# Kernel tuning notes

Hardware: AMD Instinct MI355X
Metric: run time of the kernel (lower is better)

## Reference

```python
import jax, jax.numpy as jnp
import numpy as np

L, N, HID, HEADS, BLK = 4096, 2, 1024, 16, 64
RAND_NUM = 2


def setup_inputs() -> dict:
    key = jax.random.key(0)
    ks = jax.random.split(key, 11)
    s = 0.02
    nb = L // BLK
    return {
        "query": jax.random.normal(ks[0], (L, N, HID), jnp.float32),
        "q_proj": jax.random.normal(ks[1], (HID, HID), jnp.float32) * s,
        "q_bias": jax.random.normal(ks[2], (HID,), jnp.float32) * s,
        "k_proj": jax.random.normal(ks[3], (HID, HID), jnp.float32) * s,
        "k_bias": jax.random.normal(ks[4], (HID,), jnp.float32) * s,
        "v_proj": jax.random.normal(ks[5], (HID, HID), jnp.float32) * s,
        "v_bias": jax.random.normal(ks[6], (HID,), jnp.float32) * s,
        "out_proj": jax.random.normal(ks[7], (HID, HID), jnp.float32) * s,
        "out_bias": jax.random.normal(ks[8], (HID,), jnp.float32) * s,
        "rand_indices": jax.random.randint(ks[9], (nb - 2, RAND_NUM), 2, nb, jnp.int64 if jax.config.jax_enable_x64 else jnp.int32),
        "h": HEADS,
        "block_size": BLK,
    }


def reference(query, q_proj, q_bias, k_proj, k_bias, v_proj, v_bias,
              out_proj, out_bias, rand_indices, h, block_size):
    Lq, Nb, hidden = query.shape
    dh = hidden // h
    b = block_size
    nb = Lq // b
    Z = Nb * h  # batch*heads leading dim
    scale = dh ** -0.5

    lin = lambda x, w, bi: x @ w.T + bi
    # [L, N, hidden] -> [N*h, L, dh]
    q = lin(query, q_proj, q_bias).reshape(Lq, Z, dh).transpose(1, 0, 2) * scale
    k = lin(query, k_proj, k_bias).reshape(Lq, Z, dh).transpose(1, 0, 2)
    v = lin(query, v_proj, v_bias).reshape(Lq, Z, dh).transpose(1, 0, 2)

    qb = q.reshape(Z, nb, b, dh)
    kb = k.reshape(Z, nb, b, dh)
    vb = v.reshape(Z, nb, b, dh)

    # ---- global blocks: first 2 blocks of queries attend to everything;
    #      all middle queries attend to first 2 key blocks ----
    head = jnp.einsum('zqd,zkd->zqk', q[:, :2 * b], k)          # [Z, 2b, L]
    col = jnp.einsum('zqd,zkd->zqk', q[:, 2 * b:], k[:, :2 * b])  # [Z, L-2b, 2b]

    # ---- sliding window (3 neighboring blocks), bottom row zero-padded ----
    skeys = jnp.concatenate([kb[:, 1:-2], kb[:, 2:-1], kb[:, 3:]], axis=2)  # [Z, nb-3, 3b, dh]
    sbot_k = jnp.concatenate([jnp.zeros_like(kb[:, -1:]), kb[:, -2:-1], kb[:, -1:]], axis=2)
    skeys = jnp.concatenate([skeys, sbot_k], axis=1)            # [Z, nb-2, 3b, dh]
    sqk = jnp.einsum('znqd,znkd->znqk', qb[:, 2:], skeys)
    sqk = sqk.reshape(Z, (nb - 2) * b, 3 * b)

    # ---- random blocks (rand_num per query block) ----
    gk = kb[:, rand_indices].reshape(Z, nb - 2, RAND_NUM * b, dh)
    rqk = jnp.einsum('znqd,znkd->znqk', qb[:, 2:], gk)
    rqk = rqk.reshape(Z, (nb - 2) * b, RAND_NUM * b)

    middle = jnp.concatenate([col, sqk, rqk], axis=-1)          # [Z, L-2b, 7b]

    head_attn = jax.nn.softmax(head, axis=-1)
    mid_attn = jax.nn.softmax(middle, axis=-1)

    # ---- attn @ v ----
    head_out = jnp.einsum('zqk,zkd->zqd', head_attn, v)          # [Z, 2b, dh]
    mid_out = jnp.einsum('zqk,zkd->zqd', mid_attn[:, :, :2 * b], v[:, :2 * b])

    svals = jnp.concatenate([vb[:, 1:-2], vb[:, 2:-1], vb[:, 3:]], axis=2)
    sbot_v = jnp.concatenate([vb[:, -2:-1], vb[:, -1:], jnp.zeros_like(vb[:, -1:])], axis=2)
    svals = jnp.concatenate([svals, sbot_v], axis=1)             # [Z, nb-2, 3b, dh]
    ms = mid_attn[:, :, 2 * b:5 * b].reshape(Z, nb - 2, b, 3 * b)
    mid_out = mid_out + jnp.einsum('znqk,znkd->znqd', ms, svals).reshape(Z, (nb - 2) * b, dh)

    gv = vb[:, rand_indices].reshape(Z, nb - 2, RAND_NUM * b, dh)
    mr = mid_attn[:, :, 5 * b:].reshape(Z, nb - 2, b, RAND_NUM * b)
    mid_out = mid_out + jnp.einsum('znqk,znkd->znqd', mr, gv).reshape(Z, (nb - 2) * b, dh)

    out = jnp.concatenate([head_out, mid_out], axis=1)           # [Z, L, dh]
    out = out.transpose(1, 0, 2).reshape(Lq, Nb, hidden)
    return lin(out, out_proj, out_bias)
```

## Files before the change

kernel.cpp:

```cpp
#include <hip/hip_runtime.h>
#include <stdint.h>

#define L_SEQ 4096
#define NBATCH 2
#define HID 1024
#define HEADS 16
#define DH 64
#define Z_DIM 32
#define NBLK 64
#define NROWS 8192
#define NSPLIT 8

typedef float f32x4 __attribute__((ext_vector_type(4)));
typedef short short8 __attribute__((ext_vector_type(8)));
typedef uint32_t u32x4 __attribute__((ext_vector_type(4)));

typedef const uint32_t __attribute__((address_space(1))) *gas_ptr;
typedef uint32_t __attribute__((address_space(3))) *las_ptr;

__device__ __forceinline__ ushort f2bf(float f) {
  uint32_t u = __float_as_uint(f);
  uint32_t r = (u + 0x7FFFu + ((u >> 16) & 1u)) >> 16;
  return (ushort)r;
}

__device__ __forceinline__ uint32_t cvtpk(float a, float b) {
  uint32_t r;
  asm("v_cvt_pk_bf16_f32 %0, %1, %2" : "=v"(r) : "v"(a), "v"(b));
  return r;
}

__device__ __forceinline__ void gload_lds16(const void* g, void* l) {
  __builtin_amdgcn_global_load_lds((gas_ptr)g, (las_ptr)l, 16, 0, 0);
}

__global__ __launch_bounds__(256)
void cvt_multi(const float* __restrict__ s0, ushort* __restrict__ d0,
               const float* __restrict__ s1, ushort* __restrict__ d1,
               const float* __restrict__ s2, ushort* __restrict__ d2,
               const float* __restrict__ s3, ushort* __restrict__ d3,
               const float* __restrict__ s4, ushort* __restrict__ d4) {
  const int i = blockIdx.x * blockDim.x + threadIdx.x;
  const int NQ = NROWS * HID / 4;
  const float4* src; ushort4* dst; int off;
  if (i < NQ) {
    src = (const float4*)s0; dst = (ushort4*)d0; off = i;
  } else {
    const int j = i - NQ;
    const int r = j >> 18;
    off = j & ((1 << 18) - 1);
    src = (const float4*)(r == 0 ? s1 : r == 1 ? s2 : r == 2 ? s3 : s4);
    dst = (ushort4*)(r == 0 ? d1 : r == 1 ? d2 : r == 2 ? d3 : d4);
  }
  float4 v = src[off];
  ushort4 o;
  o.x = f2bf(v.x); o.y = f2bf(v.y); o.z = f2bf(v.z); o.w = f2bf(v.w);
  dst[off] = o;
}

template <int FINAL>
__global__ __launch_bounds__(256)
void gemm_bt(const ushort* __restrict__ X,
             const ushort* __restrict__ W0, const ushort* __restrict__ W1,
             const ushort* __restrict__ W2,
             const float* __restrict__ b0, const float* __restrict__ b1,
             const float* __restrict__ b2,
             ushort* __restrict__ Qo, ushort* __restrict__ Ko,
             ushort* __restrict__ Vo, float* __restrict__ Fo) {
  const int tid = threadIdx.x;
  const int w = tid >> 6, l = tid & 63;
  const int lr = l & 15, lg = l >> 4;
  const int wr = w >> 1, wc = w & 1;

  const int total = FINAL ? 512 : 1536;
  const int per = total >> 3;
  const int f0 = blockIdx.x;
  const int nf = (f0 & 7) * per + (f0 >> 3);
  const int bx = nf & 7;
  const int by = (nf >> 3) & 63;
  const int zid = FINAL ? 0 : (nf >> 9);
  const int mbase = by * 128;
  const int nbase = bx * 128;

  const ushort* W = FINAL ? W0 : (zid == 0 ? W0 : (zid == 1 ? W1 : W2));
  const float*  B = FINAL ? b0 : (zid == 0 ? b0 : (zid == 1 ? b1 : b2));

  __shared__ ushort lds[3][8192];

  const int kch = (lg ^ ((lr >> 1) & 3)) << 3;

  f32x4 acc[4][4];
#pragma unroll
  for (int m = 0; m < 4; ++m)
#pragma unroll
    for (int n = 0; n < 4; ++n) acc[m][n] = (f32x4){0.f, 0.f, 0.f, 0.f};

  auto stage = [&](int k0, int buf) {
#pragma unroll
    for (int s = 0; s < 2; ++s) {
      const int chunk = s * 256 + tid;
      const int row = chunk >> 2, cc = chunk & 3;
      const int scc = cc ^ ((row >> 1) & 3);
      gload_lds16(X + (size_t)(mbase + row) * HID + k0 + scc * 8,
                  &lds[buf][(s * 256 + (tid & ~63)) * 8]);
      gload_lds16(W + (size_t)(nbase + row) * HID + k0 + scc * 8,
                  &lds[buf][4096 + (s * 256 + (tid & ~63)) * 8]);
    }
  };

  auto compute_tile = [&](const ushort* lA, const ushort* lB) {
    short8 af[4], bfr[4];
#pragma unroll
    for (int m = 0; m < 4; ++m)
      af[m] = *(const short8*)&lA[(wr * 64 + m * 16 + lr) * 32 + kch];
#pragma unroll
    for (int n = 0; n < 4; ++n)
      bfr[n] = *(const short8*)&lB[(wc * 64 + n * 16 + lr) * 32 + kch];
#pragma unroll
    for (int m = 0; m < 4; ++m)
#pragma unroll
      for (int n = 0; n < 4; ++n)
        acc[m][n] = __builtin_amdgcn_mfma_f32_16x16x32_bf16(af[m], bfr[n], acc[m][n], 0, 0, 0);
  };

  stage(0, 0);
  stage(32, 1);
  for (int t = 0; t < 32; ++t) {
    if (t < 30) { asm volatile("s_waitcnt vmcnt(4)" ::: "memory"); }
    else        { asm volatile("s_waitcnt vmcnt(0)" ::: "memory"); }
    __builtin_amdgcn_s_barrier();
    __builtin_amdgcn_sched_barrier(0);
    const int b = t % 3;
    compute_tile(&lds[b][0], &lds[b][4096]);
    if (t < 30) stage((t + 2) * 32, (t + 2) % 3);
  }

  if (FINAL) {
#pragma unroll
    for (int n = 0; n < 4; ++n) {
      const int col = nbase + wc * 64 + n * 16 + lr;
      const float bias = B[col];
#pragma unroll
      for (int m = 0; m < 4; ++m)
#pragma unroll
        for (int r = 0; r < 4; ++r) {
          const int row = mbase + wr * 64 + m * 16 + 4 * lg + r;
          Fo[(size_t)row * HID + col] = acc[m][n][r] + bias;
        }
    }
    return;
  }

  float biasn[4];
#pragma unroll
  for (int n = 0; n < 4; ++n) biasn[n] = B[nbase + wc * 64 + n * 16 + lr];
  ushort* st = &lds[0][0];

  if (zid == 2) {
#pragma unroll
    for (int nb2 = 0; nb2 < 2; ++nb2) {
#pragma unroll
      for (int ch = 0; ch < 2; ++ch) {
        __syncthreads();
        if (wc == ch) {
#pragma unroll
          for (int m = 0; m < 4; ++m)
#pragma unroll
            for (int n = 0; n < 4; ++n)
#pragma unroll
              for (int rr = 0; rr < 2; ++rr) {
                const int r = nb2 + 2 * rr;
                st[(n * 16 + lr) * 72 + wr * 32 + m * 8 + 2 * lg + rr] =
                    f2bf(acc[m][n][r] + biasn[n]);
              }
        }
        __syncthreads();
        const int zz = nb2 * HEADS + (nbase >> 6) + ch;
#pragma unroll
        for (int it = 0; it < 2; ++it) {
          const int c = it * 256 + tid;
          const int colI = c >> 3, ls0 = (c & 7) * 8;
          const short8 v = *(const short8*)&st[colI * 72 + ls0];
          *(short8*)&Vo[((size_t)zz * DH + colI) * L_SEQ + (mbase >> 1) + ls0] = v;
        }
      }
    }
  } else {
    ushort* Out = (zid == 0) ? Qo : Ko;
    const float sc = (zid == 0) ? 0.125f : 1.f;
#pragma unroll
    for (int nbp = 0; nbp < 2; ++nbp) {
#pragma unroll
      for (int hh = 0; hh < 2; ++hh) {
        __syncthreads();
        if (wc == hh) {
#pragma unroll
          for (int m = 0; m < 4; ++m)
#pragma unroll
            for (int n = 0; n < 4; ++n)
#pragma unroll
              for (int rr = 0; rr < 2; ++rr) {
                const int r = nbp + 2 * rr;
                st[(wr * 32 + m * 8 + 2 * lg + rr) * 72 + n * 16 + lr] =
                    f2bf((acc[m][n][r] + biasn[n]) * sc);
              }
        }
        __syncthreads();
        const int zz = nbp * HEADS + (nbase >> 6) + hh;
#pragma unroll
        for (int it = 0; it < 2; ++it) {
          const int c = it * 256 + tid;
          const int lr2 = c >> 3, cc8 = c & 7;
          const short8 v = *(const short8*)&st[lr2 * 72 + cc8 * 8];
          *(short8*)&Out[((size_t)zz * L_SEQ + (mbase >> 1) + lr2) * DH + cc8 * 8] = v;
        }
      }
    }
  }
}

__global__ __launch_bounds__(256)
void attn_sparse(const ushort* __restrict__ Q, const ushort* __restrict__ K,
                 const ushort* __restrict__ Vt, const int* __restrict__ rnd,
                 ushort* __restrict__ O,
                 float* __restrict__ Pp, float* __restrict__ Mp,
                 float* __restrict__ Lp) {
  const int bid = blockIdx.x;
  int z, qb, split = 0;
  bool head;
  if (bid < Z_DIM * 62) {
    const int x = bid & 7, k = bid >> 3;
    z = x * 4 + k / 62;
    qb = 2 + k % 62;
    head = false;
  } else {
    const int t = bid - Z_DIM * 62;
    const int x = t & 7, j = t >> 3;
    z = x * 4 + (j & 3);
    const int s2 = j >> 2;
    qb = s2 & 1;
    split = s2 >> 1;
    head = true;
  }
  const int tid = threadIdx.x;
  const int w = tid >> 6, l = tid & 63;
  const int lr = l & 15, lg = l >> 4;

  __shared__ ushort Kl[64 * 64];
  __shared__ ushort Vl[64 * 64];
  __shared__ uint32_t P2[4][16 * 36];

  const ushort* Qrow = Q + ((size_t)z * L_SEQ + qb * 64 + w * 16 + lr) * DH;
  const short8 bq0 = *(const short8*)(Qrow + lg * 8);
  const short8 bq1 = *(const short8*)(Qrow + 32 + lg * 8);

  float m = -1e30f, lsum = 0.f;
  f32x4 accO[4];
#pragma unroll
  for (int td = 0; td < 4; ++td) accO[td] = (f32x4){0.f, 0.f, 0.f, 0.f};

  const int nslot = head ? 8 : 7;
  int sk[3] = {0, 0, 0}, sv[3] = {0, 0, 0}, rk0 = 0, rk1 = 0;
  if (!head) {
    const int i = qb - 2;
    rk0 = rnd[2 * i]; rk1 = rnd[2 * i + 1];
    if (qb < NBLK - 1) {
      sk[0] = qb - 1; sk[1] = qb; sk[2] = qb + 1;
      sv[0] = qb - 1; sv[1] = qb; sv[2] = qb + 1;
    } else {
      sk[0] = -1; sk[1] = NBLK - 2; sk[2] = NBLK - 1;
      sv[0] = NBLK - 2; sv[1] = NBLK - 1; sv[2] = -1;
    }
  }

  for (int slot = 0; slot < nslot; ++slot) {
    int ki, vi;
    if (head) { ki = split * 8 + slot; vi = ki; }
    else if (slot < 2) { ki = slot; vi = slot; }
    else if (slot < 5) { ki = sk[slot - 2]; vi = sv[slot - 2]; }
    else { ki = (slot == 5) ? rk0 : rk1; vi = ki; }

    if (slot) __syncthreads();
#pragma unroll
    for (int s = 0; s < 2; ++s) {
      const int chunk = s * 256 + tid;
      const int row = chunk >> 3, cc = chunk & 7;
      const int scc = cc ^ (row & 7);
      if (ki >= 0)
        gload_lds16(K + ((size_t)z * L_SEQ + ki * 64 + row) * DH + scc * 8,
                    &Kl[(s * 256 + (tid & ~63)) * 8]);
      if (vi >= 0)
        gload_lds16(Vt + ((size_t)z * DH + row) * L_SEQ + vi * 64 + scc * 8,
                    &Vl[(s * 256 + (tid & ~63)) * 8]);
    }
    __syncthreads();

    f32x4 sc[4];
    if (ki >= 0) {
      __builtin_amdgcn_s_setprio(1);
#pragma unroll
      for (int t = 0; t < 4; ++t) {
        const int row = t * 16 + lr;
        const short8 a0 = *(const short8*)&Kl[row * 64 + ((lg ^ (row & 7)) << 3)];
        const short8 a1 = *(const short8*)&Kl[row * 64 + (((4 + lg) ^ (row & 7)) << 3)];
        f32x4 zz = (f32x4){0.f, 0.f, 0.f, 0.f};
        sc[t] = __builtin_amdgcn_mfma_f32_16x16x32_bf16(a0, bq0, zz, 0, 0, 0);
        sc[t] = __builtin_amdgcn_mfma_f32_16x16x32_bf16(a1, bq1, sc[t], 0, 0, 0);
      }
      __builtin_amdgcn_s_setprio(0);
    } else {
#pragma unroll
      for (int t = 0; t < 4; ++t) sc[t] = (f32x4){0.f, 0.f, 0.f, 0.f};
    }

    float sm = sc[0][0];
#pragma unroll
    for (int t = 0; t < 4; ++t)
#pragma unroll
      for (int r = 0; r < 4; ++r) sm = fmaxf(sm, sc[t][r]);
    sm = fmaxf(sm, __shfl_xor(sm, 16));
    sm = fmaxf(sm, __shfl_xor(sm, 32));
    const float mn = fmaxf(m, sm);
    const float scale = __expf(m - mn);
    m = mn;
    lsum *= scale;
#pragma unroll
    for (int td = 0; td < 4; ++td)
#pragma unroll
      for (int r = 0; r < 4; ++r) accO[td][r] *= scale;
    float psum = 0.f;
#pragma unroll
    for (int t = 0; t < 4; ++t)
#pragma unroll
      for (int r = 0; r < 4; ++r) {
        const float p = __expf(sc[t][r] - mn);
        sc[t][r] = p;
        psum += p;
      }
    psum += __shfl_xor(psum, 16);
    psum += __shfl_xor(psum, 32);
    lsum += psum;

    if (vi >= 0) {
      uint32_t* Pq = &P2[w][0];
#pragma unroll
      for (int t = 0; t < 4; ++t) {
        Pq[lr * 36 + t * 8 + 2 * lg + 0] = cvtpk(sc[t][0], sc[t][1]);
        Pq[lr * 36 + t * 8 + 2 * lg + 1] = cvtpk(sc[t][2], sc[t][3]);
      }
      union { u32x4 u; short8 s8; } pb0, pb1;
      pb0.u = *(const u32x4*)&Pq[lr * 36 + lg * 4];
      pb1.u = *(const u32x4*)&Pq[lr * 36 + 16 + lg * 4];
      __builtin_amdgcn_s_setprio(1);
#pragma unroll
      for (int td = 0; td < 4; ++td) {
        const int row = td * 16 + lr;
        const short8 av0 = *(const short8*)&Vl[row * 64 + ((lg ^ (row & 7)) << 3)];
        const short8 av1 = *(const short8*)&Vl[row * 64 + (((4 + lg) ^ (row & 7)) << 3)];
        accO[td] = __builtin_amdgcn_mfma_f32_16x16x32_bf16(av0, pb0.s8, accO[td], 0, 0, 0);
        accO[td] = __builtin_amdgcn_mfma_f32_16x16x32_bf16(av1, pb1.s8, accO[td], 0, 0, 0);
      }
      __builtin_amdgcn_s_setprio(0);
    }
  }

  if (!head) {
    const float inv = 1.f / lsum;
    const int nb = z >> 4, hd = z & 15;
    const size_t rowbase =
        ((size_t)(qb * 64 + w * 16 + lr) * NBATCH + nb) * HID + hd * 64;
#pragma unroll
    for (int td = 0; td < 4; ++td) {
      uint2 o;
      o.x = cvtpk(accO[td][0] * inv, accO[td][1] * inv);
      o.y = cvtpk(accO[td][2] * inv, accO[td][3] * inv);
      *(uint2*)&O[rowbase + td * 16 + 4 * lg] = o;
    }
  } else {
    const int hbase = (qb * Z_DIM + z) * NSPLIT + split;
    const size_t prow = (size_t)hbase * 64 + w * 16 + lr;
#pragma unroll
    for (int td = 0; td < 4; ++td)
      *(f32x4*)&Pp[prow * 64 + td * 16 + 4 * lg] = accO[td];
    if (l < 16) {
      Mp[hbase * 64 + w * 16 + lr] = m;
      Lp[hbase * 64 + w * 16 + lr] = lsum;
    }
  }
}

__global__ __launch_bounds__(256)
void head_reduce(const float* __restrict__ Pp, const float* __restrict__ Mp,
                 const float* __restrict__ Lp, ushort* __restrict__ O) {
  const int z = blockIdx.x >> 1, qb = blockIdx.x & 1;
  const int tid = threadIdx.x;
  const int row = tid >> 2, cg = tid & 3;
  const int base = (qb * Z_DIM + z) * NSPLIT;

  float mm[NSPLIT], wgt[NSPLIT];
  float mx = -1e30f;
#pragma unroll
  for (int s = 0; s < NSPLIT; ++s) {
    mm[s] = Mp[(base + s) * 64 + row];
    mx = fmaxf(mx, mm[s]);
  }
  float denom = 0.f;
#pragma unroll
  for (int s = 0; s < NSPLIT; ++s) {
    wgt[s] = __expf(mm[s] - mx);
    denom += Lp[(base + s) * 64 + row] * wgt[s];
  }
  const float inv = 1.f / denom;

  const int nb = z >> 4, hd = z & 15;
  const int lseq = qb * 64 + row;
#pragma unroll
  for (int c = 0; c < 16; ++c) {
    const int col = cg * 16 + c;
    float acc = 0.f;
#pragma unroll
    for (int s = 0; s < NSPLIT; ++s)
      acc += Pp[((size_t)(base + s) * 64 + row) * 64 + col] * wgt[s];
    O[((size_t)lseq * NBATCH + nb) * HID + hd * 64 + col] = f2bf(acc * inv);
  }
}

extern "C" void kernel_launch(void* const* d_in, const int* in_sizes, int n_in,
                              void* d_out, int out_size, void* d_ws, size_t ws_size,
                              hipStream_t stream) {
  (void)in_sizes; (void)n_in; (void)out_size; (void)ws_size;
  const float* query    = (const float*)d_in[0];
  const float* q_proj   = (const float*)d_in[1];
  const float* q_bias   = (const float*)d_in[2];
  const float* k_proj   = (const float*)d_in[3];
  const float* k_bias   = (const float*)d_in[4];
  const float* v_proj   = (const float*)d_in[5];
  const float* v_bias   = (const float*)d_in[6];
  const float* out_proj = (const float*)d_in[7];
  const float* out_bias = (const float*)d_in[8];
  const int*   rnd      = (const int*)d_in[9];

  ushort* Xb  = (ushort*)d_ws;
  ushort* Wq  = Xb + (size_t)NROWS * HID;
  ushort* Wk  = Wq + (size_t)HID * HID;
  ushort* Wv  = Wk + (size_t)HID * HID;
  ushort* Wo  = Wv + (size_t)HID * HID;
  ushort* Qb  = Wo + (size_t)HID * HID;
  ushort* Kb  = Qb + (size_t)Z_DIM * L_SEQ * DH;
  ushort* Vtb = Kb + (size_t)Z_DIM * L_SEQ * DH;
  float*  Pp  = (float*)(Vtb + (size_t)Z_DIM * DH * L_SEQ);
  float*  Mp  = Pp + (size_t)2 * Z_DIM * NSPLIT * 64 * 64;
  float*  Lp  = Mp + (size_t)2 * Z_DIM * NSPLIT * 64;
  ushort* Ob  = Xb;
  float*  Fo  = (float*)d_out;

  cvt_multi<<<(NROWS * HID / 4 + 4 * HID * HID / 4) / 256, 256, 0, stream>>>(
      query, Xb, q_proj, Wq, k_proj, Wk, v_proj, Wv, out_proj, Wo);

  gemm_bt<0><<<1536, 256, 0, stream>>>(
      Xb, Wq, Wk, Wv, q_bias, k_bias, v_bias, Qb, Kb, Vtb, nullptr);

  attn_sparse<<<Z_DIM * 62 + 2 * Z_DIM * NSPLIT, 256, 0, stream>>>(
      Qb, Kb, Vtb, rnd, Ob, Pp, Mp, Lp);

  head_reduce<<<2 * Z_DIM, 256, 0, stream>>>(Pp, Mp, Lp, Ob);

  gemm_bt<1><<<512, 256, 0, stream>>>(
      Ob, Wo, nullptr, nullptr, out_bias, nullptr, nullptr,
      nullptr, nullptr, nullptr, Fo);
}
```

Before: 154.6 us.

## Process two query blocks per attention workgroup to share staged K/V tiles

Each middle-region workgroup now handles two adjacent query blocks, so the global key blocks and overlapping sliding-window K/V tiles are staged once into LDS and used for both. Stages drop from 14 to 10 per pair, which cuts global-to-LDS traffic and barrier count, and the grid for that part is halved. In exchange it uses more registers for the two accumulator sets, runs fewer workgroups, and needs a special schedule for the last block pair where the padded zero-key block and the shifted value block come into play.

```diff
diff --git a/kernel.cpp b/kernel.cpp
--- a/kernel.cpp
+++ b/kernel.cpp
@@ -226,20 +226,20 @@
                  float* __restrict__ Pp, float* __restrict__ Mp,
                  float* __restrict__ Lp) {
   const int bid = blockIdx.x;
-  int z, qb, split = 0;
+  int z, p = 0, qb0 = 0, qb1 = 0, split = 0, qbh = 0;
   bool head;
-  if (bid < Z_DIM * 62) {
+  if (bid < Z_DIM * 31) {
     const int x = bid & 7, k = bid >> 3;
-    z = x * 4 + k / 62;
-    qb = 2 + k % 62;
+    z = x * 4 + k / 31;
+    p = k % 31;
+    qb0 = 2 + 2 * p; qb1 = qb0 + 1;
     head = false;
   } else {
-    const int t = bid - Z_DIM * 62;
+    const int t = bid - Z_DIM * 31;
     const int x = t & 7, j = t >> 3;
     z = x * 4 + (j & 3);
     const int s2 = j >> 2;
-    qb = s2 & 1;
-    split = s2 >> 1;
+    qbh = s2 & 1; split = s2 >> 1;
     head = true;
   }
   const int tid = threadIdx.x;
@@ -250,53 +250,45 @@
   __shared__ ushort Vl[64 * 64];
   __shared__ uint32_t P2[4][16 * 36];
 
-  const ushort* Qrow = Q + ((size_t)z * L_SEQ + qb * 64 + w * 16 + lr) * DH;
-  const short8 bq0 = *(const short8*)(Qrow + lg * 8);
-  const short8 bq1 = *(const short8*)(Qrow + 32 + lg * 8);
-
-  float m = -1e30f, lsum = 0.f;
-  f32x4 accO[4];
-#pragma unroll
-  for (int td = 0; td < 4; ++td) accO[td] = (f32x4){0.f, 0.f, 0.f, 0.f};
-
-  const int nslot = head ? 8 : 7;
-  int sk[3] = {0, 0, 0}, sv[3] = {0, 0, 0}, rk0 = 0, rk1 = 0;
+  const int qrow0 = head ? qbh : qb0;
+  const ushort* Qr0 = Q + ((size_t)z * L_SEQ + qrow0 * 64 + w * 16 + lr) * DH;
+  short8 bq0[2], bq1[2];
+  bq0[0] = *(const short8*)(Qr0 + lg * 8);
+  bq1[0] = *(const short8*)(Qr0 + 32 + lg * 8);
   if (!head) {
-    const int i = qb - 2;
-    rk0 = rnd[2 * i]; rk1 = rnd[2 * i + 1];
-    if (qb < NBLK - 1) {
-      sk[0] = qb - 1; sk[1] = qb; sk[2] = qb + 1;
-      sv[0] = qb - 1; sv[1] = qb; sv[2] = qb + 1;
-    } else {
-      sk[0] = -1; sk[1] = NBLK - 2; sk[2] = NBLK - 1;
-      sv[0] = NBLK - 2; sv[1] = NBLK - 1; sv[2] = -1;
-    }
-  }
-
-  for (int slot = 0; slot < nslot; ++slot) {
-    int ki, vi;
-    if (head) { ki = split * 8 + slot; vi = ki; }
-    else if (slot < 2) { ki = slot; vi = slot; }
-    else if (slot < 5) { ki = sk[slot - 2]; vi = sv[slot - 2]; }
-    else { ki = (slot == 5) ? rk0 : rk1; vi = ki; }
-
-    if (slot) __syncthreads();
+    const ushort* Qr1 = Q + ((size_t)z * L_SEQ + qb1 * 64 + w * 16 + lr) * DH;
+    bq0[1] = *(const short8*)(Qr1 + lg * 8);
+    bq1[1] = *(const short8*)(Qr1 + 32 + lg * 8);
+  } else {
+    bq0[1] = bq0[0]; bq1[1] = bq1[0];
+  }
+
+  float m2[2] = {-1e30f, -1e30f}, ls[2] = {0.f, 0.f};
+  f32x4 accO[2][4];
+#pragma unroll
+  for (int q = 0; q < 2; ++q)
+#pragma unroll
+    for (int td = 0; td < 4; ++td) accO[q][td] = (f32x4){0.f, 0.f, 0.f, 0.f};
+
+  auto stage = [&](int ki, int vi) {
 #pragma unroll
     for (int s = 0; s < 2; ++s) {
       const int chunk = s * 256 + tid;
       const int row = chunk >> 3, cc = chunk & 7;
       const int scc = cc ^ (row & 7);
-      if (ki >= 0)
-        gload_lds16(K + ((size_t)z * L_SEQ + ki * 64 + row) * DH + scc * 8,
-                    &Kl[(s * 256 + (tid & ~63)) * 8]);
-      if (vi >= 0)
-        gload_lds16(Vt + ((size_t)z * DH + row) * L_SEQ + vi * 64 + scc * 8,
-                    &Vl[(s * 256 + (tid & ~63)) * 8]);
-    }
-    __syncthreads();
-
+      gload_lds16(K + ((size_t)z * L_SEQ + ki * 64 + row) * DH + scc * 8,
+                  &Kl[(s * 256 + (tid & ~63)) * 8]);
+      gload_lds16(Vt + ((size_t)z * DH + row) * L_SEQ + vi * 64 + scc * 8,
+                  &Vl[(s * 256 + (tid & ~63)) * 8]);
+    }
+  };
+
+  auto process = [&](const int q, const int code) {
     f32x4 sc[4];
-    if (ki >= 0) {
+    if (code == 2) {
+#pragma unroll
+      for (int t = 0; t < 4; ++t) sc[t] = (f32x4){0.f, 0.f, 0.f, 0.f};
+    } else {
       __builtin_amdgcn_s_setprio(1);
 #pragma unroll
       for (int t = 0; t < 4; ++t) {
@@ -304,13 +296,10 @@
         const short8 a0 = *(const short8*)&Kl[row * 64 + ((lg ^ (row & 7)) << 3)];
         const short8 a1 = *(const short8*)&Kl[row * 64 + (((4 + lg) ^ (row & 7)) << 3)];
         f32x4 zz = (f32x4){0.f, 0.f, 0.f, 0.f};
-        sc[t] = __builtin_amdgcn_mfma_f32_16x16x32_bf16(a0, bq0, zz, 0, 0, 0);
-        sc[t] = __builtin_amdgcn_mfma_f32_16x16x32_bf16(a1, bq1, sc[t], 0, 0, 0);
+        sc[t] = __builtin_amdgcn_mfma_f32_16x16x32_bf16(a0, bq0[q], zz, 0, 0, 0);
+        sc[t] = __builtin_amdgcn_mfma_f32_16x16x32_bf16(a1, bq1[q], sc[t], 0, 0, 0);
       }
       __builtin_amdgcn_s_setprio(0);
-    } else {
-#pragma unroll
-      for (int t = 0; t < 4; ++t) sc[t] = (f32x4){0.f, 0.f, 0.f, 0.f};
     }
 
     float sm = sc[0][0];
@@ -320,28 +309,28 @@
       for (int r = 0; r < 4; ++r) sm = fmaxf(sm, sc[t][r]);
     sm = fmaxf(sm, __shfl_xor(sm, 16));
     sm = fmaxf(sm, __shfl_xor(sm, 32));
-    const float mn = fmaxf(m, sm);
-    const float scale = __expf(m - mn);
-    m = mn;
-    lsum *= scale;
+    const float mn = fmaxf(m2[q], sm);
+    const float scale = __expf(m2[q] - mn);
+    m2[q] = mn;
+    ls[q] *= scale;
 #pragma unroll
     for (int td = 0; td < 4; ++td)
 #pragma unroll
-      for (int r = 0; r < 4; ++r) accO[td][r] *= scale;
+      for (int r = 0; r < 4; ++r) accO[q][td][r] *= scale;
     float psum = 0.f;
 #pragma unroll
     for (int t = 0; t < 4; ++t)
 #pragma unroll
       for (int r = 0; r < 4; ++r) {
-        const float p = __expf(sc[t][r] - mn);
-        sc[t][r] = p;
-        psum += p;
+        const float pv = __expf(sc[t][r] - mn);
+        sc[t][r] = pv;
+        psum += pv;
       }
     psum += __shfl_xor(psum, 16);
     psum += __shfl_xor(psum, 32);
-    lsum += psum;
-
-    if (vi >= 0) {
+    ls[q] += psum;
+
+    if (code != 3) {
       uint32_t* Pq = &P2[w][0];
 #pragma unroll
       for (int t = 0; t < 4; ++t) {
@@ -357,34 +346,72 @@
         const int row = td * 16 + lr;
         const short8 av0 = *(const short8*)&Vl[row * 64 + ((lg ^ (row & 7)) << 3)];
         const short8 av1 = *(const short8*)&Vl[row * 64 + (((4 + lg) ^ (row & 7)) << 3)];
-        accO[td] = __builtin_amdgcn_mfma_f32_16x16x32_bf16(av0, pb0.s8, accO[td], 0, 0, 0);
-        accO[td] = __builtin_amdgcn_mfma_f32_16x16x32_bf16(av1, pb1.s8, accO[td], 0, 0, 0);
+        accO[q][td] = __builtin_amdgcn_mfma_f32_16x16x32_bf16(av0, pb0.s8, accO[q][td], 0, 0, 0);
+        accO[q][td] = __builtin_amdgcn_mfma_f32_16x16x32_bf16(av1, pb1.s8, accO[q][td], 0, 0, 0);
       }
       __builtin_amdgcn_s_setprio(0);
     }
+  };
+
+  const int nround = head ? NSPLIT : 10;
+  for (int r = 0; r < nround; ++r) {
+    int kb, vb, code0, code1;
+    if (head) {
+      kb = vb = split * 8 + r; code0 = 1; code1 = 0;
+    } else if (r < 2) {
+      kb = vb = r; code0 = 1; code1 = 1;
+    } else if (r >= 6) {
+      const bool forQ1 = (r >= 8);
+      const int ii = forQ1 ? (qb1 - 2) : (qb0 - 2);
+      kb = vb = rnd[2 * ii + (r & 1)];
+      code0 = forQ1 ? 0 : 1;
+      code1 = forQ1 ? 1 : 0;
+    } else {
+      if (p < 30) {
+        kb = vb = qb0 - 3 + r;
+        code0 = (r < 5) ? 1 : 0;
+        code1 = (r > 2) ? 1 : 0;
+      } else {
+        if (r == 2)      { kb = 61; vb = 61; code0 = 1; code1 = 0; }
+        else if (r == 3) { kb = 62; vb = 62; code0 = 1; code1 = 2; }
+        else if (r == 4) { kb = 62; vb = 63; code0 = 0; code1 = 1; }
+        else             { kb = 63; vb = 63; code0 = 1; code1 = 3; }
+      }
+    }
+
+    if (r) __syncthreads();
+    stage(kb, vb);
+    __syncthreads();
+
+    if (code0) process(0, code0);
+    if (code1) process(1, code1);
   }
 
   if (!head) {
-    const float inv = 1.f / lsum;
     const int nb = z >> 4, hd = z & 15;
-    const size_t rowbase =
-        ((size_t)(qb * 64 + w * 16 + lr) * NBATCH + nb) * HID + hd * 64;
-#pragma unroll
-    for (int td = 0; td < 4; ++td) {
-      uint2 o;
-      o.x = cvtpk(accO[td][0] * inv, accO[td][1] * inv);
-      o.y = cvtpk(accO[td][2] * inv, accO[td][3] * inv);
-      *(uint2*)&O[rowbase + td * 16 + 4 * lg] = o;
+#pragma unroll
+    for (int q = 0; q < 2; ++q) {
+      const float inv = 1.f / ls[q];
+      const int qq = q ? qb1 : qb0;
+      const size_t rowbase =
+          ((size_t)(qq * 64 + w * 16 + lr) * NBATCH + nb) * HID + hd * 64;
+#pragma unroll
+      for (int td = 0; td < 4; ++td) {
+        uint2 o;
+        o.x = cvtpk(accO[q][td][0] * inv, accO[q][td][1] * inv);
+        o.y = cvtpk(accO[q][td][2] * inv, accO[q][td][3] * inv);
+        *(uint2*)&O[rowbase + td * 16 + 4 * lg] = o;
+      }
     }
   } else {
-    const int hbase = (qb * Z_DIM + z) * NSPLIT + split;
+    const int hbase = (qbh * Z_DIM + z) * NSPLIT + split;
     const size_t prow = (size_t)hbase * 64 + w * 16 + lr;
 #pragma unroll
     for (int td = 0; td < 4; ++td)
-      *(f32x4*)&Pp[prow * 64 + td * 16 + 4 * lg] = accO[td];
+      *(f32x4*)&Pp[prow * 64 + td * 16 + 4 * lg] = accO[0][td];
     if (l < 16) {
-      Mp[hbase * 64 + w * 16 + lr] = m;
-      Lp[hbase * 64 + w * 16 + lr] = lsum;
+      Mp[hbase * 64 + w * 16 + lr] = m2[0];
+      Lp[hbase * 64 + w * 16 + lr] = ls[0];
     }
   }
 }
@@ -460,7 +487,7 @@
   gemm_bt<0><<<1536, 256, 0, stream>>>(
       Xb, Wq, Wk, Wv, q_bias, k_bias, v_bias, Qb, Kb, Vtb, nullptr);
 
-  attn_sparse<<<Z_DIM * 62 + 2 * Z_DIM * NSPLIT, 256, 0, stream>>>(
+  attn_sparse<<<Z_DIM * 31 + 2 * Z_DIM * NSPLIT, 256, 0, stream>>>(
       Qb, Kb, Vtb, rnd, Ob, Pp, Mp, Lp);
 
   head_reduce<<<2 * Z_DIM, 256, 0, stream>>>(Pp, Mp, Lp, Ob);
```

After: 155.6 us. Within noise of the previous version (+0.7%).

## Replace QKV projection GEMM with 256x256-tile, 8-wave pipelined kernel

Applied to the files above, without the earlier changes.

Adds a dedicated QKV projection kernel that uses 256x256 output tiles with 512 threads, a 64-wide K step split into two halves, and an 8-buffer LDS ring. Global-to-LDS loads are interleaved with MFMA phases, with setprio hints and explicit waitcnt/barrier scheduling. The larger tile raises arithmetic intensity and reuse of A and B per LDS load, and cuts the grid from 1536 to 384 blocks. In exchange it needs 128 KB of LDS per block and more accumulator registers, which lowers occupancy and leaves fewer blocks to balance across CUs. The old generic gemm_bt loses its QKV path and is kept only for the output projection.

```diff
diff --git a/kernel.cpp b/kernel.cpp
--- a/kernel.cpp
+++ b/kernel.cpp
@@ -58,32 +58,206 @@
   dst[off] = o;
 }
 
+#define VM4 asm volatile("s_waitcnt vmcnt(4)" ::: "memory")
+#define VMNOP
+
+#define GP(DBUF, KH, MLO, STG, VM)                                          \
+  {                                                                         \
+    const ushort* sA_ = &lds8[(DBUF) * 4 + (KH) * 2][0];                    \
+    const ushort* sB_ = &lds8[(DBUF) * 4 + (KH) * 2 + 1][0];                \
+    short8 af_[4], bf_[4];                                                  \
+    _Pragma("unroll")                                                       \
+    for (int mm = 0; mm < 4; ++mm)                                          \
+      af_[mm] = *(const short8*)&sA_[aoff + ((MLO) + mm) * 512];            \
+    _Pragma("unroll")                                                       \
+    for (int nn = 0; nn < 4; ++nn)                                          \
+      bf_[nn] = *(const short8*)&sB_[boff + nn * 512];                      \
+    STG;                                                                    \
+    VM;                                                                     \
+    __builtin_amdgcn_s_barrier();                                           \
+    asm volatile("s_waitcnt lgkmcnt(0)" ::: "memory");                      \
+    __builtin_amdgcn_sched_barrier(0);                                      \
+    __builtin_amdgcn_s_setprio(1);                                          \
+    _Pragma("unroll")                                                       \
+    for (int mm = 0; mm < 4; ++mm)                                          \
+      _Pragma("unroll")                                                     \
+      for (int nn = 0; nn < 4; ++nn)                                        \
+        acc[(MLO) + mm][nn] = __builtin_amdgcn_mfma_f32_16x16x32_bf16(      \
+            af_[mm], bf_[nn], acc[(MLO) + mm][nn], 0, 0, 0);                \
+    __builtin_amdgcn_s_setprio(0);                                          \
+    __builtin_amdgcn_s_barrier();                                           \
+  }
+
+__global__ __launch_bounds__(512)
+void gemm_qkv256(const ushort* __restrict__ X,
+                 const ushort* __restrict__ W0, const ushort* __restrict__ W1,
+                 const ushort* __restrict__ W2,
+                 const float* __restrict__ b0, const float* __restrict__ b1,
+                 const float* __restrict__ b2,
+                 ushort* __restrict__ Qo, ushort* __restrict__ Ko,
+                 ushort* __restrict__ Vo) {
+  const int tid = threadIdx.x;
+  const int w = tid >> 6, l = tid & 63;
+  const int lr = l & 15, lg = l >> 4;
+  const int wr = w >> 2, wc = w & 3;
+
+  const int f0 = blockIdx.x;
+  const int nf = (f0 & 7) * 48 + (f0 >> 3);
+  const int bx = nf & 3;
+  const int by = (nf >> 2) & 31;
+  const int zid = nf >> 7;
+  const int mbase = by * 256;
+  const int nbase = bx * 256;
+
+  const ushort* W = (zid == 0) ? W0 : (zid == 1 ? W1 : W2);
+  const float*  Bb = (zid == 0) ? b0 : (zid == 1 ? b1 : b2);
+
+  __shared__ ushort lds8[8][8192];
+
+  int srow[2], skc[2];
+#pragma unroll
+  for (int c = 0; c < 2; ++c) {
+    const int idx = c * 512 + tid;
+    const int rp = idx >> 3;
+    const int cs = (idx & 7) ^ (rp & 7);
+    srow[c] = rp * 2 + (cs >> 2);
+    skc[c] = (cs & 3) * 8;
+  }
+  const int dst0 = (tid & ~63) * 8;
+  const int dst1 = (512 + (tid & ~63)) * 8;
+
+  auto stA = [&](int dbuf, int kh, int kt) {
+    ushort* s = &lds8[dbuf * 4 + kh * 2][0];
+    const int kb = kt * 64 + kh * 32;
+    gload_lds16(X + (size_t)(mbase + srow[0]) * HID + kb + skc[0], s + dst0);
+    gload_lds16(X + (size_t)(mbase + srow[1]) * HID + kb + skc[1], s + dst1);
+  };
+  auto stB = [&](int dbuf, int kh, int kt) {
+    ushort* s = &lds8[dbuf * 4 + kh * 2 + 1][0];
+    const int kb = kt * 64 + kh * 32;
+    gload_lds16(W + (size_t)(nbase + srow[0]) * HID + kb + skc[0], s + dst0);
+    gload_lds16(W + (size_t)(nbase + srow[1]) * HID + kb + skc[1], s + dst1);
+  };
+
+  const int swz = (((lr & 1) << 2) | lg) ^ ((lr >> 1) & 7);
+  const int aoff = ((wr * 64 + (lr >> 1)) * 8 + swz) * 8;
+  const int boff = ((wc * 32 + (lr >> 1)) * 8 + swz) * 8;
+
+  f32x4 acc[8][4];
+#pragma unroll
+  for (int m = 0; m < 8; ++m)
+#pragma unroll
+    for (int n = 0; n < 4; ++n) acc[m][n] = (f32x4){0.f, 0.f, 0.f, 0.f};
+
+  stA(0, 0, 0); stB(0, 0, 0);
+  stA(0, 1, 0); stB(0, 1, 0);
+  stA(1, 0, 1); stB(1, 0, 1);
+  asm volatile("s_waitcnt vmcnt(4)" ::: "memory");
+  __builtin_amdgcn_s_barrier();
+
+  for (int i = 0; i < 8; ++i) {
+    const int ka = 2 * i + 1;
+    const int kb2 = (2 * i + 2 > 15) ? 15 : (2 * i + 2);
+    const int kc3 = (2 * i + 3 > 15) ? 15 : (2 * i + 3);
+    GP(0, 0, 0, stA(1, 1, ka), VMNOP);
+    GP(0, 0, 4, stB(1, 1, ka), VMNOP);
+    GP(0, 1, 0, stA(0, 0, kb2), VMNOP);
+    GP(0, 1, 4, stB(0, 0, kb2), VM4);
+    GP(1, 0, 0, stA(0, 1, kb2), VMNOP);
+    GP(1, 0, 4, stB(0, 1, kb2), VMNOP);
+    GP(1, 1, 0, stA(1, 0, kc3), VMNOP);
+    GP(1, 1, 4, stB(1, 0, kc3), VM4);
+  }
+  asm volatile("s_waitcnt vmcnt(0)" ::: "memory");
+  __builtin_amdgcn_s_barrier();
+
+  float biasn[4];
+#pragma unroll
+  for (int n = 0; n < 4; ++n) biasn[n] = Bb[nbase + wc * 64 + n * 16 + lr];
+  ushort* slab = &lds8[0][0];
+
+  if (zid == 2) {
+#pragma unroll
+    for (int nb2 = 0; nb2 < 2; ++nb2) {
+#pragma unroll
+      for (int ch = 0; ch < 4; ++ch) {
+        __builtin_amdgcn_s_barrier();
+        if (wc == ch) {
+#pragma unroll
+          for (int m = 0; m < 8; ++m)
+#pragma unroll
+            for (int n = 0; n < 4; ++n)
+#pragma unroll
+              for (int rr = 0; rr < 2; ++rr) {
+                const int r = nb2 + 2 * rr;
+                const int ls = wr * 64 + m * 8 + 2 * lg + rr;
+                slab[(n * 16 + lr) * 136 + ls] = f2bf(acc[m][n][r] + biasn[n]);
+              }
+        }
+        __builtin_amdgcn_s_barrier();
+        const int zz = nb2 * HEADS + bx * 4 + ch;
+#pragma unroll
+        for (int it = 0; it < 2; ++it) {
+          const int c = it * 512 + tid;
+          const int colI = c >> 4, chk = c & 15;
+          const short8 v = *(const short8*)&slab[colI * 136 + chk * 8];
+          *(short8*)&Vo[((size_t)zz * DH + colI) * L_SEQ + (mbase >> 1) + chk * 8] = v;
+        }
+      }
+    }
+  } else {
+    ushort* Out = (zid == 0) ? Qo : Ko;
+    const float sc = (zid == 0) ? 0.125f : 1.f;
+#pragma unroll
+    for (int nbp = 0; nbp < 2; ++nbp) {
+      __builtin_amdgcn_s_barrier();
+#pragma unroll
+      for (int m = 0; m < 8; ++m)
+#pragma unroll
+        for (int n = 0; n < 4; ++n)
+#pragma unroll
+          for (int rr = 0; rr < 2; ++rr) {
+            const int r = nbp + 2 * rr;
+            const int ls = wr * 64 + m * 8 + 2 * lg + rr;
+            slab[ls * 264 + wc * 64 + n * 16 + lr] =
+                f2bf((acc[m][n][r] + biasn[n]) * sc);
+          }
+      __builtin_amdgcn_s_barrier();
+#pragma unroll
+      for (int it = 0; it < 8; ++it) {
+        const int c = it * 512 + tid;
+        const int ls2 = c >> 5, ck = c & 31;
+        const int col = ck * 8;
+        const short8 v = *(const short8*)&slab[ls2 * 264 + col];
+        const int zz = nbp * HEADS + bx * 4 + (col >> 6);
+        *(short8*)&Out[((size_t)zz * L_SEQ + (mbase >> 1) + ls2) * DH + (col & 63)] = v;
+      }
+    }
+  }
+}
+
 template <int FINAL>
 __global__ __launch_bounds__(256)
 void gemm_bt(const ushort* __restrict__ X,
-             const ushort* __restrict__ W0, const ushort* __restrict__ W1,
-             const ushort* __restrict__ W2,
-             const float* __restrict__ b0, const float* __restrict__ b1,
-             const float* __restrict__ b2,
-             ushort* __restrict__ Qo, ushort* __restrict__ Ko,
-             ushort* __restrict__ Vo, float* __restrict__ Fo) {
+             const ushort* __restrict__ W0,
+             const float* __restrict__ b0,
+             float* __restrict__ Fo) {
   const int tid = threadIdx.x;
   const int w = tid >> 6, l = tid & 63;
   const int lr = l & 15, lg = l >> 4;
   const int wr = w >> 1, wc = w & 1;
 
-  const int total = FINAL ? 512 : 1536;
+  const int total = 512;
   const int per = total >> 3;
   const int f0 = blockIdx.x;
   const int nf = (f0 & 7) * per + (f0 >> 3);
   const int bx = nf & 7;
   const int by = (nf >> 3) & 63;
-  const int zid = FINAL ? 0 : (nf >> 9);
   const int mbase = by * 128;
   const int nbase = bx * 128;
 
-  const ushort* W = FINAL ? W0 : (zid == 0 ? W0 : (zid == 1 ? W1 : W2));
-  const float*  B = FINAL ? b0 : (zid == 0 ? b0 : (zid == 1 ? b1 : b2));
+  const ushort* W = W0;
+  const float*  B = b0;
 
   __shared__ ushort lds[3][8192];
 
@@ -135,87 +309,17 @@
     if (t < 30) stage((t + 2) * 32, (t + 2) % 3);
   }
 
-  if (FINAL) {
-#pragma unroll
-    for (int n = 0; n < 4; ++n) {
-      const int col = nbase + wc * 64 + n * 16 + lr;
-      const float bias = B[col];
-#pragma unroll
-      for (int m = 0; m < 4; ++m)
-#pragma unroll
-        for (int r = 0; r < 4; ++r) {
-          const int row = mbase + wr * 64 + m * 16 + 4 * lg + r;
-          Fo[(size_t)row * HID + col] = acc[m][n][r] + bias;
-        }
-    }
-    return;
-  }
-
-  float biasn[4];
-#pragma unroll
-  for (int n = 0; n < 4; ++n) biasn[n] = B[nbase + wc * 64 + n * 16 + lr];
-  ushort* st = &lds[0][0];
-
-  if (zid == 2) {
-#pragma unroll
-    for (int nb2 = 0; nb2 < 2; ++nb2) {
-#pragma unroll
-      for (int ch = 0; ch < 2; ++ch) {
-        __syncthreads();
-        if (wc == ch) {
-#pragma unroll
-          for (int m = 0; m < 4; ++m)
-#pragma unroll
-            for (int n = 0; n < 4; ++n)
-#pragma unroll
-              for (int rr = 0; rr < 2; ++rr) {
-                const int r = nb2 + 2 * rr;
-                st[(n * 16 + lr) * 72 + wr * 32 + m * 8 + 2 * lg + rr] =
-                    f2bf(acc[m][n][r] + biasn[n]);
-              }
-        }
-        __syncthreads();
-        const int zz = nb2 * HEADS + (nbase >> 6) + ch;
-#pragma unroll
-        for (int it = 0; it < 2; ++it) {
-          const int c = it * 256 + tid;
-          const int colI = c >> 3, ls0 = (c & 7) * 8;
-          const short8 v = *(const short8*)&st[colI * 72 + ls0];
-          *(short8*)&Vo[((size_t)zz * DH + colI) * L_SEQ + (mbase >> 1) + ls0] = v;
-        }
-      }
-    }
-  } else {
-    ushort* Out = (zid == 0) ? Qo : Ko;
-    const float sc = (zid == 0) ? 0.125f : 1.f;
-#pragma unroll
-    for (int nbp = 0; nbp < 2; ++nbp) {
-#pragma unroll
-      for (int hh = 0; hh < 2; ++hh) {
-        __syncthreads();
-        if (wc == hh) {
-#pragma unroll
-          for (int m = 0; m < 4; ++m)
-#pragma unroll
-            for (int n = 0; n < 4; ++n)
-#pragma unroll
-              for (int rr = 0; rr < 2; ++rr) {
-                const int r = nbp + 2 * rr;
-                st[(wr * 32 + m * 8 + 2 * lg + rr) * 72 + n * 16 + lr] =
-                    f2bf((acc[m][n][r] + biasn[n]) * sc);
-              }
-        }
-        __syncthreads();
-        const int zz = nbp * HEADS + (nbase >> 6) + hh;
-#pragma unroll
-        for (int it = 0; it < 2; ++it) {
-          const int c = it * 256 + tid;
-          const int lr2 = c >> 3, cc8 = c & 7;
-          const short8 v = *(const short8*)&st[lr2 * 72 + cc8 * 8];
-          *(short8*)&Out[((size_t)zz * L_SEQ + (mbase >> 1) + lr2) * DH + cc8 * 8] = v;
-        }
-      }
-    }
+#pragma unroll
+  for (int n = 0; n < 4; ++n) {
+    const int col = nbase + wc * 64 + n * 16 + lr;
+    const float bias = B[col];
+#pragma unroll
+    for (int m = 0; m < 4; ++m)
+#pragma unroll
+      for (int r = 0; r < 4; ++r) {
+        const int row = mbase + wr * 64 + m * 16 + 4 * lg + r;
+        Fo[(size_t)row * HID + col] = acc[m][n][r] + bias;
+      }
   }
 }
 
@@ -457,15 +561,13 @@
   cvt_multi<<<(NROWS * HID / 4 + 4 * HID * HID / 4) / 256, 256, 0, stream>>>(
       query, Xb, q_proj, Wq, k_proj, Wk, v_proj, Wv, out_proj, Wo);
 
-  gemm_bt<0><<<1536, 256, 0, stream>>>(
-      Xb, Wq, Wk, Wv, q_bias, k_bias, v_bias, Qb, Kb, Vtb, nullptr);
+  gemm_qkv256<<<384, 512, 0, stream>>>(
+      Xb, Wq, Wk, Wv, q_bias, k_bias, v_bias, Qb, Kb, Vtb);
 
   attn_sparse<<<Z_DIM * 62 + 2 * Z_DIM * NSPLIT, 256, 0, stream>>>(
       Qb, Kb, Vtb, rnd, Ob, Pp, Mp, Lp);
 
   head_reduce<<<2 * Z_DIM, 256, 0, stream>>>(Pp, Mp, Lp, Ob);
 
-  gemm_bt<1><<<512, 256, 0, stream>>>(
-      Ob, Wo, nullptr, nullptr, out_bias, nullptr, nullptr,
-      nullptr, nullptr, nullptr, Fo);
-}
+  gemm_bt<1><<<512, 256, 0, stream>>>(Ob, Wo, out_bias, Fo);
+}
```

New measurement: 160.0 us. +3.5%, slower.
